# Performance work log

Hardware: AMD Instinct MI355X
Metric: run time of the kernel (lower is better)

The kernel has to match this reference:

```python
import jax, jax.numpy as jnp
import numpy as np

T, S, F = 256, 128, 1024  # t frames, s persons, person_feature_len (= attn_len)


def setup_inputs() -> dict:
    key = jax.random.key(0)
    ks = jax.random.split(key, 9)
    scale = 1.0 / np.sqrt(F)
    return {
        "batch_data": jax.random.normal(ks[0], (T * S, F), dtype=jnp.float32),
        "xywh": jax.random.uniform(ks[1], (T * S, 4), dtype=jnp.float32),
        "Wa": jax.random.normal(ks[2], (F, F), dtype=jnp.float32) * scale,
        "ba": jnp.zeros((F,), dtype=jnp.float32),
        "Wb": jax.random.normal(ks[3], (F, F), dtype=jnp.float32) * scale,
        "bb": jnp.zeros((F,), dtype=jnp.float32),
        "Wg": jax.random.normal(ks[4], (F, F), dtype=jnp.float32) * scale,
        "bg": jnp.zeros((F,), dtype=jnp.float32),
        "OW": 1280,
        "OH": 720,
        "num_person": jax.random.randint(ks[5], (T,), 0, S, dtype=jnp.int64),
    }


def reference(batch_data, xywh, Wa, ba, Wb, bb, Wg, bg, OW, OH, num_person):
    # SemPosBlock.forward: only the SpatioVisualModule path contributes to the output.
    x = batch_data.reshape(T, S, F)            # person features per frame
    theta = jnp.einsum("tsf,fa->tsa", x, Wa) + ba
    phi = jnp.einsum("tsf,fa->tsa", x, Wb) + bb
    feats = jnp.einsum("tsf,fa->tsa", x, Wg) + bg
    # per-frame person-person attention: softmax(theta @ phi^T) @ feats
    scores = jnp.einsum("tsa,tja->tsj", theta, phi)     # [T, S, S]
    weights = jax.nn.softmax(scores, axis=-1)
    results = jnp.einsum("tsj,tja->tsa", weights, feats)  # [T, S, F]
    return results
```

## Files before the change

kernel.cpp:

```cpp
#include <hip/hip_runtime.h>

typedef _Float16 f16x8 __attribute__((ext_vector_type(8)));
typedef __attribute__((ext_vector_type(4))) float f32x4;

__device__ __forceinline__ unsigned short f16b(float x){
  _Float16 h = (_Float16)x;
  return __builtin_bit_cast(unsigned short, h);
}
__device__ __forceinline__ void split2h(float x, unsigned short &hi, unsigned short &lo){
  _Float16 h = (_Float16)x;
  _Float16 l = (_Float16)(x - (float)h);
  hi = __builtin_bit_cast(unsigned short, h);
  lo = __builtin_bit_cast(unsigned short, l);
}
__device__ __forceinline__ void gload_lds16(const void* g, void* l){
  __builtin_amdgcn_global_load_lds((const __attribute__((address_space(1))) void*)g,
                                   (__attribute__((address_space(3))) void*)l, 16, 0, 0);
}
#define VM(N)    asm volatile("s_waitcnt vmcnt(" #N ")" ::: "memory")
#define LGKM0()  do { asm volatile("s_waitcnt lgkmcnt(0)" ::: "memory"); \
                      __builtin_amdgcn_sched_barrier(0); } while(0)
#define BAR()    do { __builtin_amdgcn_s_barrier(); \
                      __builtin_amdgcn_sched_barrier(0); } while(0)

template<int NK, int EPI>
__device__ __forceinline__ void gemm_body(
    const unsigned short* __restrict__ A, const unsigned short* __restrict__ B,
    unsigned short* __restrict__ outp, const float* __restrict__ bias,
    int lda, int ldb, int bm, int bn, char* ldsb)
{
  const int tid  = threadIdx.x;
  const int w    = tid >> 6;
  const int lane = tid & 63;
  const int wm   = w >> 2;
  const int wn   = w & 3;
  const int l15  = lane & 15;
  const int lg   = lane >> 4;

  int srow[2], slg[2];
#pragma unroll
  for (int j = 0; j < 2; j++){
    int o16 = j * 512 + tid;
    int p = o16 >> 3, s = o16 & 7;
    int q = s ^ (p & 7);
    srow[j] = 2 * p + (q >> 2);
    slg[j]  = q & 3;
  }
  const unsigned short* aS0 = A + (size_t)(bm * 256 + srow[0]) * lda + slg[0] * 8;
  const unsigned short* aS1 = A + (size_t)(bm * 256 + srow[1]) * lda + slg[1] * 8;
  const unsigned short* bS0 = B + (size_t)(bn * 256 + srow[0]) * ldb + slg[0] * 8;
  const unsigned short* bS1 = B + (size_t)(bn * 256 + srow[1]) * ldb + slg[1] * 8;

  const int sA   = (((l15 & 1) << 2) | lg) ^ ((l15 >> 1) & 7);
  const int rps  = (l15 >> 1) * 128 + sA * 16;

  f32x4 acc[8][4];
  f32x4 zero = {0.f, 0.f, 0.f, 0.f};
#pragma unroll
  for (int m = 0; m < 8; m++)
#pragma unroll
    for (int n = 0; n < 4; n++) acc[m][n] = zero;

  auto STAGE_Q = [&](int t, int q){
    char* slot = ldsb + (size_t)(t & 1) * 65536;
    const int kb = t * 64;
    if (q == 0){
      gload_lds16(aS0 + kb,      slot +         w * 1024);
      gload_lds16(aS1 + kb,      slot +  8192 + w * 1024);
    } else if (q == 1){
      gload_lds16(bS0 + kb,      slot + 32768 + w * 1024);
      gload_lds16(bS1 + kb,      slot + 40960 + w * 1024);
    } else if (q == 2){
      gload_lds16(bS0 + kb + 32, slot + 49152 + w * 1024);
      gload_lds16(bS1 + kb + 32, slot + 57344 + w * 1024);
    } else {
      gload_lds16(aS0 + kb + 32, slot + 16384 + w * 1024);
      gload_lds16(aS1 + kb + 32, slot + 24576 + w * 1024);
    }
  };

  STAGE_Q(0, 0); STAGE_Q(0, 1); STAGE_Q(0, 2); STAGE_Q(0, 3);

#pragma unroll 1
  for (int t = 0; t < NK; t++){
    const char* sb = ldsb + (size_t)(t & 1) * 65536;
    const bool pre = (t + 1 < NK);
    f16x8 aF[4], bF[4], aG[4], bF2[4], aF2[4], aG2[4];

    VM(4);
    BAR();
    if (pre) STAGE_Q(t + 1, 0);
#pragma unroll
    for (int m = 0; m < 4; m++) aF[m] = *(const f16x8*)(sb + wm * 8192 + m * 1024 + rps);
#pragma unroll
    for (int n = 0; n < 4; n++) bF[n] = *(const f16x8*)(sb + 32768 + wn * 4096 + n * 1024 + rps);
    LGKM0();
    __builtin_amdgcn_s_setprio(1);
#pragma unroll
    for (int m = 0; m < 4; m++)
#pragma unroll
      for (int n = 0; n < 4; n++)
        acc[m][n] = __builtin_amdgcn_mfma_f32_16x16x32_f16(aF[m], bF[n], acc[m][n], 0, 0, 0);
    __builtin_amdgcn_s_setprio(0);
    if (pre) STAGE_Q(t + 1, 1);
#pragma unroll
    for (int m = 0; m < 4; m++) aG[m] = *(const f16x8*)(sb + wm * 8192 + (m + 4) * 1024 + rps);
    LGKM0();
    __builtin_amdgcn_s_setprio(1);
#pragma unroll
    for (int m = 0; m < 4; m++)
#pragma unroll
      for (int n = 0; n < 4; n++)
        acc[m + 4][n] = __builtin_amdgcn_mfma_f32_16x16x32_f16(aG[m], bF[n], acc[m + 4][n], 0, 0, 0);
    __builtin_amdgcn_s_setprio(0);

    if (pre) { VM(4); } else { VM(0); }
    BAR();
    if (pre) STAGE_Q(t + 1, 2);
#pragma unroll
    for (int m = 0; m < 4; m++) aF2[m] = *(const f16x8*)(sb + 16384 + wm * 8192 + m * 1024 + rps);
#pragma unroll
    for (int n = 0; n < 4; n++) bF2[n] = *(const f16x8*)(sb + 49152 + wn * 4096 + n * 1024 + rps);
    LGKM0();
    __builtin_amdgcn_s_setprio(1);
#pragma unroll
    for (int m = 0; m < 4; m++)
#pragma unroll
      for (int n = 0; n < 4; n++)
        acc[m][n] = __builtin_amdgcn_mfma_f32_16x16x32_f16(aF2[m], bF2[n], acc[m][n], 0, 0, 0);
    __builtin_amdgcn_s_setprio(0);
    if (pre) STAGE_Q(t + 1, 3);
#pragma unroll
    for (int m = 0; m < 4; m++) aG2[m] = *(const f16x8*)(sb + 16384 + wm * 8192 + (m + 4) * 1024 + rps);
    LGKM0();
    __builtin_amdgcn_s_setprio(1);
#pragma unroll
    for (int m = 0; m < 4; m++)
#pragma unroll
      for (int n = 0; n < 4; n++)
        acc[m + 4][n] = __builtin_amdgcn_mfma_f32_16x16x32_f16(aG2[m], bF2[n], acc[m + 4][n], 0, 0, 0);
    __builtin_amdgcn_s_setprio(0);
  }

#pragma unroll
  for (int m = 0; m < 8; m++)
#pragma unroll
    for (int n = 0; n < 4; n++){
      const int col  = bn * 256 + wn * 64 + n * 16 + l15;
      const int row0 = bm * 256 + wm * 128 + m * 16 + lg * 4;
      if (EPI == 4){
#pragma unroll
        for (int q = 0; q < 4; q++)
          outp[(size_t)(row0 + q) * 2048 + col] = f16b(acc[m][n][q]);
      } else if (EPI == 6){
        float* of = (float*)outp;
#pragma unroll
        for (int q = 0; q < 4; q++)
          of[(size_t)col * 1024 + row0 + q] = acc[m][n][q];
      } else if (EPI == 7){
#pragma unroll
        for (int q = 0; q < 4; q++)
          outp[(size_t)(row0 + q) * 32768 + col] = f16b(acc[m][n][q] + bias[row0 + q]);
      }
    }
}

__global__ __launch_bounds__(512, 2) void k_big(
    const unsigned short* __restrict__ x2, const unsigned short* __restrict__ MTh,
    unsigned short* __restrict__ y2, const unsigned short* __restrict__ WgTh,
    unsigned short* __restrict__ FT, const float* __restrict__ bg)
{
  __shared__ __align__(16) unsigned short lds_u[65536];
  const int b = blockIdx.x;
  int k = b >> 1;
  k = (k & 7) * 64 + (k >> 3);
  if ((b & 1) == 0){
    gemm_body<16, 4>(x2, MTh, y2, nullptr, 1024, 1024, k >> 2, k & 3, (char*)lds_u);
  } else {
    gemm_body<16, 7>(WgTh, x2, FT, bg, 1024, 1024, k & 3, k >> 2, (char*)lds_u);
  }
}

__global__ __launch_bounds__(512, 1) void k_mtx(
    const unsigned short* __restrict__ Wa2, const unsigned short* __restrict__ Wb2,
    float* __restrict__ Mpart,
    const float* __restrict__ x, unsigned short* __restrict__ x2,
    const float* __restrict__ wv, float* __restrict__ v)
{
  __shared__ __align__(16) unsigned short lds_u[65536];
  const int b = blockIdx.x;
  if (b < 96){
    const int s = b >> 5, rest = b & 31;
    const int kc = rest >> 4, tile = rest & 15;
    const unsigned short* Aa = Wa2 + (s == 1 ? 1024 : 0) + kc * 512;
    const unsigned short* Bb = Wb2 + (s == 2 ? 1024 : 0) + kc * 512;
    gemm_body<8, 6>(Aa, Bb, (unsigned short*)(Mpart + (size_t)(s * 2 + kc) * 1048576),
                    nullptr, 2048, 2048, tile >> 2, tile & 3, (char*)lds_u);
  } else {
    const int bb = b - 96;
    const int w = threadIdx.x >> 6, lane = threadIdx.x & 63;
#pragma unroll
    for (int it = 0; it < 4; it++){
      const int row = bb * 8 + w + it * 8192;
      float s = 0.f;
#pragma unroll
      for (int j = 0; j < 4; j++){
        const int c = lane * 4 + j * 256;
        float4 val = *(const float4*)(x + (size_t)row * 1024 + c);
        float4 wvv = *(const float4*)(wv + c);
        ushort4 h, l;
        split2h(val.x, h.x, l.x); split2h(val.y, h.y, l.y);
        split2h(val.z, h.z, l.z); split2h(val.w, h.w, l.w);
        *(ushort4*)(x2 + (size_t)row * 1024 + c) = h;
        s += val.x * wvv.x + val.y * wvv.y + val.z * wvv.z + val.w * wvv.w;
      }
      for (int o = 32; o; o >>= 1) s += __shfl_xor(s, o);
      if (lane == 0) v[row] = s;
    }
  }
}

__global__ __launch_bounds__(256) void k_mt_reduce(const float* __restrict__ P,
                                                   unsigned short* __restrict__ MTh){
  const size_t i = ((size_t)blockIdx.x * 256 + threadIdx.x) * 4;
  float4 s = *(const float4*)(P + i);
#pragma unroll
  for (int p = 1; p < 6; p++){
    float4 a = *(const float4*)(P + (size_t)p * 1048576 + i);
    s.x += a.x; s.y += a.y; s.z += a.z; s.w += a.w;
  }
  ushort4 h;
  h.x = f16b(s.x); h.y = f16b(s.y); h.z = f16b(s.z); h.w = f16b(s.w);
  *(ushort4*)(MTh + i) = h;
}

__global__ __launch_bounds__(1024) void k_frame(
    const unsigned short* Y2, const unsigned short* X2,
    const float* __restrict__ v, const unsigned short* __restrict__ FT,
    float* outp)
{
  __shared__ __align__(16) unsigned short lds_u[49152];
  char* ldsb = (char*)lds_u;

  const int frame = blockIdx.x;
  const int tid  = threadIdx.x;
  const int w    = tid >> 6;
  const int lane = tid & 63;
  const int wm   = w >> 2;
  const int wn   = w & 3;
  const int l15  = lane & 15;
  const int lg   = lane >> 4;

  const int cS = tid & 511, hS = tid >> 9;
  const int pS = cS >> 3, sS = cS & 7;
  const int qS = sS ^ (pS & 7);
  const int srow = 2 * pS + (qS >> 2);
  const int slg  = qS & 3;
  const unsigned short* yS = Y2 + (size_t)(frame * 128 + srow) * 2048 + slg * 8;
  const unsigned short* xS = X2 + (size_t)(frame * 128 + srow) * 1024 + slg * 8;
  const int dY =         hS * 8192 + cS * 16;
  const int dX = 16384 + hS * 8192 + cS * 16;

  const int sA  = (((l15 & 1) << 2) | lg) ^ ((l15 >> 1) & 7);
  const int rps = (l15 >> 1) * 128 + sA * 16;

  f32x4 acc[2][2];
  f32x4 zero = {0.f, 0.f, 0.f, 0.f};
#pragma unroll
  for (int m = 0; m < 2; m++)
#pragma unroll
    for (int n = 0; n < 2; n++) acc[m][n] = zero;

  auto STAGE_K = [&](int t){
    char* slot = ldsb + (size_t)(t & 1) * 32768;
    const int kk = t * 64 + hS * 32;
    gload_lds16(yS + kk, slot + dY);
    gload_lds16(xS + kk, slot + dX);
  };

  const int NK = 16;
  STAGE_K(0);

#pragma unroll 1
  for (int t = 0; t < NK; t++){
    const char* sb = ldsb + (size_t)(t & 1) * 32768;
    if (t + 1 < NK){ STAGE_K(t + 1); VM(2); } else { VM(0); }
    BAR();
    f16x8 aF[2][2], bh[2][2];
#pragma unroll
    for (int h = 0; h < 2; h++){
#pragma unroll
      for (int m = 0; m < 2; m++)
        aF[h][m] = *(const f16x8*)(sb + h * 8192 + (wm * 2 + m) * 1024 + rps);
#pragma unroll
      for (int n = 0; n < 2; n++)
        bh[h][n] = *(const f16x8*)(sb + 16384 + h * 8192 + (wn * 2 + n) * 1024 + rps);
    }
    LGKM0();
    __builtin_amdgcn_s_setprio(1);
#pragma unroll
    for (int h = 0; h < 2; h++)
#pragma unroll
      for (int m = 0; m < 2; m++)
#pragma unroll
        for (int n = 0; n < 2; n++)
          acc[m][n] = __builtin_amdgcn_mfma_f32_16x16x32_f16(aF[h][m], bh[h][n], acc[m][n], 0, 0, 0);
    __builtin_amdgcn_s_setprio(0);
    BAR();
  }

  BAR();
  float* sf = (float*)ldsb;
#pragma unroll
  for (int m = 0; m < 2; m++)
#pragma unroll
    for (int n = 0; n < 2; n++){
      const int col = wn * 32 + n * 16 + l15;
#pragma unroll
      for (int q = 0; q < 4; q++){
        const int row = wm * 32 + m * 16 + lg * 4 + q;
        sf[row * 128 + ((col + (row & 31) * 4) & 127)] = acc[m][n][q];
      }
    }
  LGKM0(); BAR();
  unsigned short* Pb = (unsigned short*)(ldsb + 65536);
  {
    const float* vr = v + (size_t)frame * 128;
#pragma unroll 1
    for (int i = 0; i < 8; i++){
      const int row = w * 8 + i;
      const float* rp = sf + row * 128;
      const int rot = (row & 31) * 4;
      float a = rp[(lane + rot) & 127]      + vr[lane];
      float b = rp[(lane + 64 + rot) & 127] + vr[lane + 64];
      float mx = fmaxf(a, b);
      for (int o = 32; o; o >>= 1) mx = fmaxf(mx, __shfl_xor(mx, o));
      float ea = __expf(a - mx), eb = __expf(b - mx);
      float s = ea + eb;
      for (int o = 32; o; o >>= 1) s += __shfl_xor(s, o);
      const float inv = 1.0f / s;
      unsigned short* prow = (unsigned short*)((char*)Pb + row * 256);
      const int j0 = lane, j1 = lane + 64;
      *(unsigned short*)((char*)prow + (((j0 >> 3) ^ (row & 15)) * 16) + (j0 & 7) * 2) = f16b(ea * inv);
      *(unsigned short*)((char*)prow + (((j1 >> 3) ^ (row & 15)) * 16) + (j1 & 7) * 2) = f16b(eb * inv);
    }
  }
  LGKM0(); BAR();

  char* Fb = ldsb;
  auto STAGE_F = [&](int h){
    char* slot = Fb + (size_t)(h & 1) * 32768;
#pragma unroll
    for (int j = 0; j < 2; j++){
      const int o = j * 1024 + tid;
      const int a = o >> 4, c = o & 15;
      gload_lds16(FT + (size_t)(h * 128 + a) * 32768 + frame * 128 + (c ^ (a & 15)) * 8,
                  slot + (size_t)o * 16);
    }
  };
  STAGE_F(0);

#pragma unroll 1
  for (int h = 0; h < 8; h++){
    if (h + 1 < 8){ STAGE_F(h + 1); VM(2); } else { VM(0); }
    BAR();
    const char* fs = Fb + (size_t)(h & 1) * 32768;
    f16x8 pF[4][2], fF[4][2];
#pragma unroll
    for (int ks = 0; ks < 4; ks++){
#pragma unroll
      for (int m = 0; m < 2; m++){
        const int row = wm * 32 + m * 16 + l15;
        pF[ks][m] = *(const f16x8*)((char*)Pb + row * 256 + (((ks * 4 + lg) ^ (row & 15)) * 16));
      }
#pragma unroll
      for (int n = 0; n < 2; n++){
        const int al = wn * 32 + n * 16 + l15;
        fF[ks][n] = *(const f16x8*)(fs + al * 256 + (((ks * 4 + lg) ^ (al & 15)) * 16));
      }
    }
    LGKM0();
    f32x4 accP[2][2];
#pragma unroll
    for (int m = 0; m < 2; m++)
#pragma unroll
      for (int n = 0; n < 2; n++) accP[m][n] = zero;
    __builtin_amdgcn_s_setprio(1);
#pragma unroll
    for (int ks = 0; ks < 4; ks++)
#pragma unroll
      for (int m = 0; m < 2; m++)
#pragma unroll
        for (int n = 0; n < 2; n++)
          accP[m][n] = __builtin_amdgcn_mfma_f32_16x16x32_f16(pF[ks][m], fF[ks][n], accP[m][n], 0, 0, 0);
    __builtin_amdgcn_s_setprio(0);
#pragma unroll
    for (int m = 0; m < 2; m++)
#pragma unroll
      for (int n = 0; n < 2; n++){
        const int f  = h * 128 + wn * 32 + n * 16 + l15;
        const int r0 = wm * 32 + m * 16 + lg * 4;
#pragma unroll
        for (int q = 0; q < 4; q++)
          outp[((size_t)frame * 128 + r0 + q) * 1024 + f] = accP[m][n][q];
      }
    BAR();
  }
}

__global__ __launch_bounds__(256) void k_prep(const float* __restrict__ Wa,
                                              const float* __restrict__ Wb,
                                              const float* __restrict__ Wg,
                                              const float* __restrict__ ba,
                                              unsigned short* __restrict__ Wa2,
                                              unsigned short* __restrict__ Wb2,
                                              unsigned short* __restrict__ WgTh,
                                              float* __restrict__ wv){
  const int b = blockIdx.x;
  if (b < 2048){
    const int row = (b < 1024) ? b : (b - 1024);
    const float* src = (b < 1024) ? Wa : Wb;
    unsigned short* dst = (b < 1024) ? Wa2 : Wb2;
    const int c = threadIdx.x * 4;
    float4 val = *(const float4*)(src + (size_t)row * 1024 + c);
    ushort4 h, l;
    split2h(val.x, h.x, l.x); split2h(val.y, h.y, l.y);
    split2h(val.z, h.z, l.z); split2h(val.w, h.w, l.w);
    *(ushort4*)(dst + (size_t)row * 2048 + c) = h;
    *(ushort4*)(dst + (size_t)row * 2048 + 1024 + c) = l;
  } else if (b < 3072){
    const int row = b - 2048;
    const int c0 = threadIdx.x * 4;
    float4 val = *(const float4*)(Wg + (size_t)row * 1024 + c0);
    float vv[4] = {val.x, val.y, val.z, val.w};
#pragma unroll
    for (int i = 0; i < 4; i++)
      WgTh[(size_t)(c0 + i) * 1024 + row] = f16b(vv[i]);
  } else {
    const int row = (b - 3072) * 4 + (threadIdx.x >> 6);
    const int lane = threadIdx.x & 63;
    float s = 0.f;
#pragma unroll
    for (int j = 0; j < 4; j++){
      const int c = lane * 4 + j * 256;
      float4 wb = *(const float4*)(Wb + (size_t)row * 1024 + c);
      float4 bb = *(const float4*)(ba + c);
      s += wb.x * bb.x + wb.y * bb.y + wb.z * bb.z + wb.w * bb.w;
    }
    for (int o = 32; o; o >>= 1) s += __shfl_xor(s, o);
    if (lane == 0) wv[row] = s;
  }
}

extern "C" void kernel_launch(void* const* d_in, const int* in_sizes, int n_in,
                              void* d_out, int out_size, void* d_ws, size_t ws_size,
                              hipStream_t stream) {
  const float* x  = (const float*)d_in[0];
  const float* Wa = (const float*)d_in[2];
  const float* ba = (const float*)d_in[3];
  const float* Wb = (const float*)d_in[4];
  const float* Wg = (const float*)d_in[6];
  const float* bg = (const float*)d_in[7];

  unsigned short* x2   = (unsigned short*)d_ws;
  unsigned short* Wa2  = x2 + (size_t)32768 * 1024;
  unsigned short* Wb2  = Wa2 + (size_t)1024 * 2048;
  unsigned short* WgTh = Wb2 + (size_t)1024 * 2048;
  unsigned short* MTh  = WgTh + (size_t)1024 * 1024;
  unsigned short* FT   = MTh + (size_t)1024 * 1024;
  float* Mpart = (float*)(FT + (size_t)1024 * 32768);
  float* wv = Mpart + (size_t)6 * 1048576;
  float* v  = wv + 1024;
  size_t need = (size_t)((char*)(v + 32768) - (char*)d_ws);
  if (ws_size < need) return;

  unsigned short* y2 = (unsigned short*)d_out;

  k_prep      <<<3328, 256, 0, stream>>>(Wa, Wb, Wg, ba, Wa2, Wb2, WgTh, wv);
  k_mtx       <<<1120, 512, 0, stream>>>(Wa2, Wb2, Mpart, x, x2, wv, v);
  k_mt_reduce <<<1024, 256, 0, stream>>>(Mpart, MTh);
  k_big       <<<1024, 512, 0, stream>>>(x2, MTh, y2, WgTh, FT, bg);
  k_frame     <<<256, 1024, 0, stream>>>(y2, x2, v, FT, (float*)d_out);
}
```

Before: 273.1 us.

## Use K=32 double-buffered GEMM body in k_big to halve LDS footprint

```diff
diff --git a/kernel.cpp b/kernel.cpp
--- a/kernel.cpp
+++ b/kernel.cpp
@@ -148,16 +148,94 @@
     for (int n = 0; n < 4; n++){
       const int col  = bn * 256 + wn * 64 + n * 16 + l15;
       const int row0 = bm * 256 + wm * 128 + m * 16 + lg * 4;
+      float* of = (float*)outp;
+#pragma unroll
+      for (int q = 0; q < 4; q++)
+        of[(size_t)col * 1024 + row0 + q] = acc[m][n][q];
+    }
+}
+
+template<int NK, int EPI>
+__device__ __forceinline__ void gemm_body32(
+    const unsigned short* __restrict__ A, const unsigned short* __restrict__ B,
+    unsigned short* __restrict__ outp, const float* __restrict__ bias,
+    int lda, int ldb, int bm, int bn, char* ldsb)
+{
+  const int tid  = threadIdx.x;
+  const int w    = tid >> 6;
+  const int lane = tid & 63;
+  const int wm   = w >> 2;
+  const int wn   = w & 3;
+  const int l15  = lane & 15;
+  const int lg   = lane >> 4;
+
+  int srow[2], slg[2];
+#pragma unroll
+  for (int j = 0; j < 2; j++){
+    int o16 = j * 512 + tid;
+    int p = o16 >> 3, s = o16 & 7;
+    int q = s ^ (p & 7);
+    srow[j] = 2 * p + (q >> 2);
+    slg[j]  = q & 3;
+  }
+  const unsigned short* aS0 = A + (size_t)(bm * 256 + srow[0]) * lda + slg[0] * 8;
+  const unsigned short* aS1 = A + (size_t)(bm * 256 + srow[1]) * lda + slg[1] * 8;
+  const unsigned short* bS0 = B + (size_t)(bn * 256 + srow[0]) * ldb + slg[0] * 8;
+  const unsigned short* bS1 = B + (size_t)(bn * 256 + srow[1]) * ldb + slg[1] * 8;
+
+  const int sA   = (((l15 & 1) << 2) | lg) ^ ((l15 >> 1) & 7);
+  const int rps  = (l15 >> 1) * 128 + sA * 16;
+
+  f32x4 acc[8][4];
+  f32x4 zero = {0.f, 0.f, 0.f, 0.f};
+#pragma unroll
+  for (int m = 0; m < 8; m++)
+#pragma unroll
+    for (int n = 0; n < 4; n++) acc[m][n] = zero;
+
+  auto STAGE_T = [&](int t){
+    char* slot = ldsb + (size_t)(t & 1) * 32768;
+    const int kb = t * 32;
+    gload_lds16(aS0 + kb, slot +         w * 1024);
+    gload_lds16(aS1 + kb, slot +  8192 + w * 1024);
+    gload_lds16(bS0 + kb, slot + 16384 + w * 1024);
+    gload_lds16(bS1 + kb, slot + 24576 + w * 1024);
+  };
+
+  STAGE_T(0);
+
+#pragma unroll 1
+  for (int t = 0; t < NK; t++){
+    const char* sb = ldsb + (size_t)(t & 1) * 32768;
+    VM(0);
+    BAR();
+    if (t + 1 < NK) STAGE_T(t + 1);
+    f16x8 aF[8], bF[4];
+#pragma unroll
+    for (int m = 0; m < 8; m++) aF[m] = *(const f16x8*)(sb + wm * 8192 + m * 1024 + rps);
+#pragma unroll
+    for (int n = 0; n < 4; n++) bF[n] = *(const f16x8*)(sb + 16384 + wn * 4096 + n * 1024 + rps);
+    LGKM0();
+    __builtin_amdgcn_s_setprio(1);
+#pragma unroll
+    for (int m = 0; m < 8; m++)
+#pragma unroll
+      for (int n = 0; n < 4; n++)
+        acc[m][n] = __builtin_amdgcn_mfma_f32_16x16x32_f16(aF[m], bF[n], acc[m][n], 0, 0, 0);
+    __builtin_amdgcn_s_setprio(0);
+  }
+
+#pragma unroll
+  for (int m = 0; m < 8; m++)
+#pragma unroll
+    for (int n = 0; n < 4; n++){
+      const int col  = bn * 256 + wn * 64 + n * 16 + l15;
+      const int row0 = bm * 256 + wm * 128 + m * 16 + lg * 4;
       if (EPI == 4){
 #pragma unroll
         for (int q = 0; q < 4; q++)
           outp[(size_t)(row0 + q) * 2048 + col] = f16b(acc[m][n][q]);
-      } else if (EPI == 6){
-        float* of = (float*)outp;
-#pragma unroll
-        for (int q = 0; q < 4; q++)
-          of[(size_t)col * 1024 + row0 + q] = acc[m][n][q];
-      } else if (EPI == 7){
+      } else {
 #pragma unroll
         for (int q = 0; q < 4; q++)
           outp[(size_t)(row0 + q) * 32768 + col] = f16b(acc[m][n][q] + bias[row0 + q]);
@@ -170,14 +248,14 @@
     unsigned short* __restrict__ y2, const unsigned short* __restrict__ WgTh,
     unsigned short* __restrict__ FT, const float* __restrict__ bg)
 {
-  __shared__ __align__(16) unsigned short lds_u[65536];
+  __shared__ __align__(16) unsigned short lds_u[32768];
   const int b = blockIdx.x;
   int k = b >> 1;
   k = (k & 7) * 64 + (k >> 3);
   if ((b & 1) == 0){
-    gemm_body<16, 4>(x2, MTh, y2, nullptr, 1024, 1024, k >> 2, k & 3, (char*)lds_u);
+    gemm_body32<32, 4>(x2, MTh, y2, nullptr, 1024, 1024, k >> 2, k & 3, (char*)lds_u);
   } else {
-    gemm_body<16, 7>(WgTh, x2, FT, bg, 1024, 1024, k & 3, k >> 2, (char*)lds_u);
+    gemm_body32<32, 7>(WgTh, x2, FT, bg, 1024, 1024, k & 3, k >> 2, (char*)lds_u);
   }
 }
 
```

After: 276.1 us. No clear change (+1.1%).
